# Optimization experiments

Hardware: AMD Instinct MI355X
Metric: run time of the kernel (lower is better)

## Reference

```python
import jax, jax.numpy as jnp
import numpy as np

B, S, E = 8, 4096, 768
NEG = jnp.float32(-1e30)


def setup_inputs() -> dict:
    key = jax.random.key(0)
    ks = jax.random.split(key, 9)
    full_ebd = jax.random.normal(ks[0], (B, S, E), dtype=jnp.float32)
    # first_idx in [64, S//2): end of question span (question tokens are 1..first_idx-1)
    first = jax.random.randint(ks[1], (B,), 64, S // 2)
    # second_idx in (first, S): end of context span (unused by the math but part of API)
    second = jax.random.randint(ks[2], (B,), S // 2 + 1, S)
    SEQ_idxes = jnp.stack([first, second], axis=1).astype(jnp.int64)
    w = 0.02
    Wq_w = jax.random.normal(ks[3], (E, E), dtype=jnp.float32) * w
    Wq_b = jax.random.normal(ks[4], (E,), dtype=jnp.float32) * w
    Wk_w = jax.random.normal(ks[5], (E, E), dtype=jnp.float32) * w
    Wk_b = jax.random.normal(ks[6], (E,), dtype=jnp.float32) * w
    Wv_w = jax.random.normal(ks[7], (E, E), dtype=jnp.float32) * w
    Wv_b = jax.random.normal(ks[8], (E,), dtype=jnp.float32) * w
    return {"full_ebd": full_ebd, "SEQ_idxes": SEQ_idxes,
            "Wq_w": Wq_w, "Wq_b": Wq_b, "Wk_w": Wk_w, "Wk_b": Wk_b,
            "Wv_w": Wv_w, "Wv_b": Wv_b}


def reference(full_ebd, SEQ_idxes, Wq_w, Wq_b, Wk_w, Wk_b, Wv_w, Wv_b):
    # Vectorized form of the ragged per-sample loop: queries attend to the
    # question tokens 1..first_idx-1 only; masking keys reproduces the slice.
    seq = full_ebd.shape[1]
    inv_sqrt_dk = jnp.float32(1.0 / np.sqrt(full_ebd.shape[-1]))
    Q = full_ebd @ Wq_w.T + Wq_b              # [B,S,E]
    K = full_ebd @ Wk_w.T + Wk_b              # [B,S,E]
    V = full_ebd @ Wv_w.T + Wv_b              # [B,S,E]
    first = SEQ_idxes[:, 0]                   # [B]
    j = jnp.arange(seq)
    key_mask = (j[None, :] >= 1) & (j[None, :] < first[:, None])  # [B,S]
    scores = jnp.einsum('bqe,bke->bqk', Q, K) * inv_sqrt_dk       # [B,S,S]
    scores = jnp.where(key_mask[:, None, :], scores, NEG)
    attn = jax.nn.softmax(scores, axis=-1)
    attn = attn * key_mask[:, None, :].astype(attn.dtype)  # exact zeros outside span
    H = jnp.einsum('bqk,bke->bqe', attn, V)   # [B,S,E]
    return H
```

## Files before the change

kernel.cpp:

```cpp
#include <hip/hip_runtime.h>
#include <hip/hip_bf16.h>
#include <cmath>

typedef __bf16 bf16x8 __attribute__((ext_vector_type(8)));
typedef __bf16 bf16x4 __attribute__((ext_vector_type(4)));
typedef float f32x4 __attribute__((ext_vector_type(4)));

#define GLOBAL_AS __attribute__((address_space(1)))
#define LDS_AS __attribute__((address_space(3)))

__device__ __forceinline__ void async_copy16(const void* g, void* l) {
    __builtin_amdgcn_global_load_lds((const GLOBAL_AS void*)g, (LDS_AS void*)l, 16, 0, 0);
}

__device__ inline int get_first(const int* __restrict__ seq, int b) {
    int stride = (seq[1] == 0) ? 4 : 2;
    return seq[b * stride];
}

__global__ __launch_bounds__(256) void cast_f32_bf16(const float* __restrict__ in,
                                                     __bf16* __restrict__ out, int n4) {
    int i = blockIdx.x * 256 + threadIdx.x;
    if (i >= n4) return;
    float4 v = ((const float4*)in)[i];
    bf16x4 o;
    o[0] = (__bf16)v.x; o[1] = (__bf16)v.y; o[2] = (__bf16)v.z; o[3] = (__bf16)v.w;
    ((bf16x4*)out)[i] = o;
}

__global__ __launch_bounds__(256) void cast3_f32_bf16(
    const float* __restrict__ a, const float* __restrict__ b, const float* __restrict__ c,
    __bf16* __restrict__ oa, __bf16* __restrict__ ob, __bf16* __restrict__ oc, int n4) {
    int i = blockIdx.x * 256 + threadIdx.x;
    if (i >= n4) return;
    const float* in = (blockIdx.y == 0) ? a : (blockIdx.y == 1) ? b : c;
    __bf16* out = (blockIdx.y == 0) ? oa : (blockIdx.y == 1) ? ob : oc;
    float4 v = ((const float4*)in)[i];
    bf16x4 o;
    o[0] = (__bf16)v.x; o[1] = (__bf16)v.y; o[2] = (__bf16)v.z; o[3] = (__bf16)v.w;
    ((bf16x4*)out)[i] = o;
}

__global__ __launch_bounds__(256) void zero_f32(float* __restrict__ p, int n4) {
    int i = blockIdx.x * 256 + threadIdx.x;
    if (i < n4) ((f32x4*)p)[i] = f32x4{0.f, 0.f, 0.f, 0.f};
}

template <int EPI>
__global__ __launch_bounds__(256) void gemm_bt(
    const __bf16* __restrict__ A, int lda, long strideA,
    const __bf16* __restrict__ B, int ldb, long strideB,
    const float* __restrict__ bias,
    void* __restrict__ Cv, int ldc, long strideC,
    int Kfix, const int* __restrict__ seq, int exit_mode, int k_mode,
    float cs, float* __restrict__ rowsum) {
    int z = blockIdx.z;
    int m0 = blockIdx.x * 128, n0 = blockIdx.y * 128;
    int first = seq ? get_first(seq, z) : 0;
    if (exit_mode == 1 && m0 >= first) return;
    if (exit_mode == 2 && n0 >= first) return;
    int K = k_mode ? ((first + 63) & ~63) : Kfix;

    __shared__ char As[16384];
    __shared__ char Bs[16384];

    int tid = threadIdx.x;
    int lane = tid & 63, wid = tid >> 6;
    int waveM = (wid & 1) << 6, waveN = (wid >> 1) << 6;
    int quad = lane >> 4, l16 = lane & 15;

    int r0 = tid >> 3;
    int c8 = (tid & 7) ^ (r0 & 7);
    const __bf16* Ag = A + (long)z * strideA + (long)(m0 + r0) * lda + c8 * 8;
    const __bf16* Bg = B + (long)z * strideB + (long)(n0 + r0) * ldb + c8 * 8;

    f32x4 acc[4][4] = {};
    int xorv = (l16 & 7) << 4;

    for (int k0 = 0; k0 < K; k0 += 64) {
        __syncthreads();
#pragma unroll
        for (int r = 0; r < 4; ++r) {
            async_copy16(Ag + (long)(r * 32) * lda + k0, As + (tid + r * 256) * 16);
            async_copy16(Bg + (long)(r * 32) * ldb + k0, Bs + (tid + r * 256) * 16);
        }
        __syncthreads();
#pragma unroll
        for (int s = 0; s < 2; ++s) {
            bf16x8 af[4], bfr[4];
#pragma unroll
            for (int i = 0; i < 4; ++i) {
                int chunk = (((s << 2) + quad) << 4) ^ xorv;
                af[i]  = *(const bf16x8*)(As + (waveM + i * 16 + l16) * 128 + chunk);
                bfr[i] = *(const bf16x8*)(Bs + (waveN + i * 16 + l16) * 128 + chunk);
            }
#pragma unroll
            for (int i = 0; i < 4; ++i)
#pragma unroll
                for (int j = 0; j < 4; ++j)
                    acc[i][j] = __builtin_amdgcn_mfma_f32_16x16x32_bf16(af[i], bfr[j], acc[i][j], 0, 0, 0);
        }
    }

    if (EPI == 0) {
        __bf16* C = (__bf16*)Cv + (long)z * strideC;
#pragma unroll
        for (int i = 0; i < 4; ++i) {
            int rowb = m0 + waveM + i * 16 + quad * 4;
#pragma unroll
            for (int j = 0; j < 4; ++j) {
                int col = n0 + waveN + j * 16 + l16;
                float bv_ = bias[col];
#pragma unroll
                for (int r = 0; r < 4; ++r)
                    C[(long)(rowb + r) * ldc + col] = (__bf16)(acc[i][j][r] + bv_);
            }
        }
    } else if (EPI == 1) {
        __bf16* C = (__bf16*)Cv + (long)z * strideC;
#pragma unroll
        for (int i = 0; i < 4; ++i) {
            int rowb = m0 + waveM + i * 16 + quad * 4;
#pragma unroll
            for (int j = 0; j < 4; ++j) {
                int col = n0 + waveN + j * 16 + l16;
                float bv_ = bias[col];
                bf16x4 o;
#pragma unroll
                for (int r = 0; r < 4; ++r) o[r] = (__bf16)(acc[i][j][r] + bv_);
                *(bf16x4*)&C[(long)col * ldc + rowb] = o;
            }
        }
    } else if (EPI == 2) {
        __bf16* C = (__bf16*)Cv + (long)z * strideC;
        float* rs = rowsum + (long)z * 4096;
#pragma unroll
        for (int i = 0; i < 4; ++i) {
            int rowb = m0 + waveM + i * 16 + quad * 4;
            float sum[4] = {0.f, 0.f, 0.f, 0.f};
#pragma unroll
            for (int j = 0; j < 4; ++j) {
                int col = n0 + waveN + j * 16 + l16;
                bool valid = (col >= 1) && (col < first);
#pragma unroll
                for (int r = 0; r < 4; ++r) {
                    float e = valid ? exp2f(acc[i][j][r] * cs) : 0.0f;
                    __bf16 pb = (__bf16)e;
                    C[(long)(rowb + r) * ldc + col] = pb;
                    sum[r] += (float)pb;
                }
            }
#pragma unroll
            for (int r = 0; r < 4; ++r) {
                float v = sum[r];
                v += __shfl_xor(v, 8); v += __shfl_xor(v, 4);
                v += __shfl_xor(v, 2); v += __shfl_xor(v, 1);
                if (l16 == 0) atomicAdd(&rs[rowb + r], v);
            }
        }
    } else {
        float* C = (float*)Cv + (long)z * strideC;
        const float* rs = rowsum + (long)z * 4096;
#pragma unroll
        for (int i = 0; i < 4; ++i) {
            int rowb = m0 + waveM + i * 16 + quad * 4;
            float inv[4];
#pragma unroll
            for (int r = 0; r < 4; ++r) inv[r] = 1.0f / rs[rowb + r];
#pragma unroll
            for (int j = 0; j < 4; ++j) {
                int col = n0 + waveN + j * 16 + l16;
#pragma unroll
                for (int r = 0; r < 4; ++r)
                    C[(long)(rowb + r) * ldc + col] = acc[i][j][r] * inv[r];
            }
        }
    }
}

extern "C" void kernel_launch(void* const* d_in, const int* in_sizes, int n_in,
                              void* d_out, int out_size, void* d_ws, size_t ws_size,
                              hipStream_t stream) {
    const int B = 8, S = 4096, E = 768, SK = 2048;
    const float* ebd  = (const float*)d_in[0];
    const int*   seq  = (const int*)d_in[1];
    const float* Wq_w = (const float*)d_in[2];
    const float* Wq_b = (const float*)d_in[3];
    const float* Wk_w = (const float*)d_in[4];
    const float* Wk_b = (const float*)d_in[5];
    const float* Wv_w = (const float*)d_in[6];
    const float* Wv_b = (const float*)d_in[7];
    float* out = (float*)d_out;

    char* p = (char*)d_ws;
    __bf16* ebd_bf = (__bf16*)p; p += (size_t)B * S * E * 2;
    __bf16* wq = (__bf16*)p;     p += (size_t)E * E * 2;
    __bf16* wk = (__bf16*)p;     p += (size_t)E * E * 2;
    __bf16* wv = (__bf16*)p;     p += (size_t)E * E * 2;
    __bf16* Qb = (__bf16*)p;     p += (size_t)B * S * E * 2;
    __bf16* Kb = (__bf16*)p;     p += (size_t)B * SK * E * 2;
    __bf16* VT = (__bf16*)p;     p += (size_t)B * E * SK * 2;
    __bf16* Pb = (__bf16*)p;     p += (size_t)B * S * SK * 2;
    float* rowsum = (float*)p;   p += (size_t)B * S * 4;

    zero_f32<<<B * S / 4 / 256, 256, 0, stream>>>(rowsum, B * S / 4);
    cast_f32_bf16<<<(B * S * E / 4 + 255) / 256, 256, 0, stream>>>(ebd, ebd_bf, B * S * E / 4);
    cast3_f32_bf16<<<dim3((E * E / 4 + 255) / 256, 3), 256, 0, stream>>>(
        Wq_w, Wk_w, Wv_w, wq, wk, wv, E * E / 4);

    float cs = (1.0f / sqrtf((float)E)) * 1.44269504088896f;

    gemm_bt<0><<<dim3(B * S / 128, E / 128, 1), 256, 0, stream>>>(
        ebd_bf, E, 0, wq, E, 0, Wq_b, Qb, E, 0, E, nullptr, 0, 0, 0.f, nullptr);
    gemm_bt<0><<<dim3(SK / 128, E / 128, B), 256, 0, stream>>>(
        ebd_bf, E, (long)S * E, wk, E, 0, Wk_b, Kb, E, (long)SK * E, E, seq, 1, 0, 0.f, nullptr);
    gemm_bt<1><<<dim3(SK / 128, E / 128, B), 256, 0, stream>>>(
        ebd_bf, E, (long)S * E, wv, E, 0, Wv_b, VT, SK, (long)E * SK, E, seq, 1, 0, 0.f, nullptr);
    gemm_bt<2><<<dim3(S / 128, SK / 128, B), 256, 0, stream>>>(
        Qb, E, (long)S * E, Kb, E, (long)SK * E, nullptr, Pb, SK, (long)S * SK, E, seq, 2, 0, cs, rowsum);
    gemm_bt<3><<<dim3(S / 128, E / 128, B), 256, 0, stream>>>(
        Pb, SK, (long)S * SK, VT, SK, (long)E * SK, nullptr, out, E, (long)S * E, 0, seq, 0, 1, 0.f, rowsum);
}
```

Baseline: 450.1 us.

## Add 256x256 eight-wave GEMM with interleaved staging for Q, scores and PV

```diff
diff --git a/kernel.cpp b/kernel.cpp
--- a/kernel.cpp
+++ b/kernel.cpp
@@ -12,6 +12,9 @@
 __device__ __forceinline__ void async_copy16(const void* g, void* l) {
     __builtin_amdgcn_global_load_lds((const GLOBAL_AS void*)g, (LDS_AS void*)l, 16, 0, 0);
 }
+
+#define SBAR() asm volatile("s_barrier" ::: "memory")
+#define WAITLGKM0() asm volatile("s_waitcnt lgkmcnt(0)" ::: "memory")
 
 __device__ inline int get_first(const int* __restrict__ seq, int b) {
     int stride = (seq[1] == 0) ? 4 : 2;
@@ -116,7 +119,7 @@
                     C[(long)(rowb + r) * ldc + col] = (__bf16)(acc[i][j][r] + bv_);
             }
         }
-    } else if (EPI == 1) {
+    } else {
         __bf16* C = (__bf16*)Cv + (long)z * strideC;
 #pragma unroll
         for (int i = 0; i < 4; ++i) {
@@ -131,16 +134,170 @@
                 *(bf16x4*)&C[(long)col * ldc + rowb] = o;
             }
         }
+    }
+}
+
+template <int EPI>
+__global__ __launch_bounds__(512, 2) void gemm256(
+    const __bf16* __restrict__ A, int lda, long strideA,
+    const __bf16* __restrict__ B, int ldb, long strideB,
+    const float* __restrict__ bias,
+    void* __restrict__ Cv, int ldc, long strideC,
+    int Kfix, const int* __restrict__ seq, int exit_mode, int k_mode,
+    float cs, float* __restrict__ rowsum) {
+    int z = blockIdx.z;
+    int m0 = blockIdx.x * 256, n0 = blockIdx.y * 256;
+    int first = seq ? get_first(seq, z) : 0;
+    if (exit_mode == 2 && n0 >= first) return;
+    int K = k_mode ? ((first + 63) & ~63) : Kfix;
+    int nt = K >> 6;
+
+    __shared__ char As[2][32768];
+    __shared__ char Bs[2][32768];
+
+    int tid = threadIdx.x;
+    int lane = tid & 63, wid = tid >> 6;
+    int wr = (wid >> 2) << 7;
+    int wc = (wid & 3) << 6;
+    int quad = lane >> 4, l16 = lane & 15;
+    int xr = l16 & 7;
+
+    int rg = tid >> 3;
+    int src_c8 = (tid & 7) ^ (rg & 7);
+    const __bf16* Ag = A + (long)z * strideA + (long)(m0 + rg) * lda + src_c8 * 8;
+    const __bf16* Bg = B + (long)z * strideB + (long)(n0 + rg) * ldb + src_c8 * 8;
+
+#define STAGE_A(bb, g, kk) async_copy16(Ag + (long)((g) * 64) * lda + (kk), &As[bb][(g) * 8192 + tid * 16])
+#define STAGE_B(bb, g, kk) async_copy16(Bg + (long)((g) * 64) * ldb + (kk), &Bs[bb][(g) * 8192 + tid * 16])
+#define AFRAG(base, row, s) (*(const bf16x8*)((base) + (row) * 128 + ((((s << 2) + quad) ^ xr) << 4)))
+
+    f32x4 acc[8][4] = {};
+
+    STAGE_A(0, 0, 0); STAGE_A(0, 2, 0);
+    STAGE_B(0, 0, 0); STAGE_B(0, 2, 0);
+    STAGE_B(0, 1, 0); STAGE_B(0, 3, 0);
+    STAGE_A(0, 1, 0); STAGE_A(0, 3, 0);
+    asm volatile("s_waitcnt vmcnt(2)" ::: "memory");
+    SBAR();
+
+    bf16x8 a[4][2];
+    bf16x8 bq[2][2][2];
+
+    for (int kt = 0; kt < nt; ++kt) {
+        int buf = kt & 1, nbuf = buf ^ 1;
+        int k0n = (kt + 1) << 6;
+        bool stg = (kt + 1) < nt;
+        const char* Ab = &As[buf][0];
+        const char* Bb = &Bs[buf][0];
+
+#pragma unroll
+        for (int i = 0; i < 4; ++i)
+#pragma unroll
+            for (int s = 0; s < 2; ++s)
+                a[i][s] = AFRAG(Ab, wr + i * 16 + l16, s);
+#pragma unroll
+        for (int j = 0; j < 2; ++j)
+#pragma unroll
+            for (int s = 0; s < 2; ++s)
+                bq[0][j][s] = AFRAG(Bb, wc + j * 16 + l16, s);
+        if (stg) { STAGE_A(nbuf, 0, k0n); STAGE_A(nbuf, 2, k0n); STAGE_B(nbuf, 0, k0n); STAGE_B(nbuf, 2, k0n); }
+        SBAR();
+        WAITLGKM0();
+        __builtin_amdgcn_s_setprio(1);
+#pragma unroll
+        for (int i = 0; i < 4; ++i)
+#pragma unroll
+            for (int j = 0; j < 2; ++j)
+#pragma unroll
+                for (int s = 0; s < 2; ++s)
+                    acc[i][j] = __builtin_amdgcn_mfma_f32_16x16x32_bf16(a[i][s], bq[0][j][s], acc[i][j], 0, 0, 0);
+        __builtin_amdgcn_s_setprio(0);
+        SBAR();
+
+#pragma unroll
+        for (int j = 0; j < 2; ++j)
+#pragma unroll
+            for (int s = 0; s < 2; ++s)
+                bq[1][j][s] = AFRAG(Bb, wc + 32 + j * 16 + l16, s);
+        if (stg) {
+            STAGE_B(nbuf, 1, k0n); STAGE_B(nbuf, 3, k0n);
+            STAGE_A(nbuf, 1, k0n); STAGE_A(nbuf, 3, k0n);
+            asm volatile("s_waitcnt vmcnt(8)" ::: "memory");
+        } else {
+            asm volatile("s_waitcnt vmcnt(0)" ::: "memory");
+        }
+        SBAR();
+        WAITLGKM0();
+        __builtin_amdgcn_s_setprio(1);
+#pragma unroll
+        for (int i = 0; i < 4; ++i)
+#pragma unroll
+            for (int j = 0; j < 2; ++j)
+#pragma unroll
+                for (int s = 0; s < 2; ++s)
+                    acc[i][2 + j] = __builtin_amdgcn_mfma_f32_16x16x32_bf16(a[i][s], bq[1][j][s], acc[i][2 + j], 0, 0, 0);
+        __builtin_amdgcn_s_setprio(0);
+        SBAR();
+
+#pragma unroll
+        for (int i = 0; i < 4; ++i)
+#pragma unroll
+            for (int s = 0; s < 2; ++s)
+                a[i][s] = AFRAG(Ab, wr + 64 + i * 16 + l16, s);
+        SBAR();
+        WAITLGKM0();
+        __builtin_amdgcn_s_setprio(1);
+#pragma unroll
+        for (int i = 0; i < 4; ++i)
+#pragma unroll
+            for (int j = 0; j < 2; ++j)
+#pragma unroll
+                for (int s = 0; s < 2; ++s)
+                    acc[4 + i][j] = __builtin_amdgcn_mfma_f32_16x16x32_bf16(a[i][s], bq[0][j][s], acc[4 + i][j], 0, 0, 0);
+        __builtin_amdgcn_s_setprio(0);
+        SBAR();
+
+        asm volatile("s_waitcnt vmcnt(2)" ::: "memory");
+        SBAR();
+        __builtin_amdgcn_s_setprio(1);
+#pragma unroll
+        for (int i = 0; i < 4; ++i)
+#pragma unroll
+            for (int j = 0; j < 2; ++j)
+#pragma unroll
+                for (int s = 0; s < 2; ++s)
+                    acc[4 + i][2 + j] = __builtin_amdgcn_mfma_f32_16x16x32_bf16(a[i][s], bq[1][j][s], acc[4 + i][2 + j], 0, 0, 0);
+        __builtin_amdgcn_s_setprio(0);
+        SBAR();
+    }
+#undef STAGE_A
+#undef STAGE_B
+#undef AFRAG
+
+    if (EPI == 0) {
+        __bf16* C = (__bf16*)Cv + (long)z * strideC;
+#pragma unroll
+        for (int i = 0; i < 8; ++i) {
+            int rowb = m0 + wr + i * 16 + quad * 4;
+#pragma unroll
+            for (int j = 0; j < 4; ++j) {
+                int col = n0 + wc + j * 16 + l16;
+                float bv_ = bias[col];
+#pragma unroll
+                for (int r = 0; r < 4; ++r)
+                    C[(long)(rowb + r) * ldc + col] = (__bf16)(acc[i][j][r] + bv_);
+            }
+        }
     } else if (EPI == 2) {
         __bf16* C = (__bf16*)Cv + (long)z * strideC;
-        float* rs = rowsum + (long)z * 4096;
-#pragma unroll
-        for (int i = 0; i < 4; ++i) {
-            int rowb = m0 + waveM + i * 16 + quad * 4;
+        float* rsum = rowsum + (long)z * 4096;
+#pragma unroll
+        for (int i = 0; i < 8; ++i) {
+            int rowb = m0 + wr + i * 16 + quad * 4;
             float sum[4] = {0.f, 0.f, 0.f, 0.f};
 #pragma unroll
             for (int j = 0; j < 4; ++j) {
-                int col = n0 + waveN + j * 16 + l16;
+                int col = n0 + wc + j * 16 + l16;
                 bool valid = (col >= 1) && (col < first);
 #pragma unroll
                 for (int r = 0; r < 4; ++r) {
@@ -155,21 +312,21 @@
                 float v = sum[r];
                 v += __shfl_xor(v, 8); v += __shfl_xor(v, 4);
                 v += __shfl_xor(v, 2); v += __shfl_xor(v, 1);
-                if (l16 == 0) atomicAdd(&rs[rowb + r], v);
+                if (l16 == 0) atomicAdd(&rsum[rowb + r], v);
             }
         }
     } else {
         float* C = (float*)Cv + (long)z * strideC;
-        const float* rs = rowsum + (long)z * 4096;
-#pragma unroll
-        for (int i = 0; i < 4; ++i) {
-            int rowb = m0 + waveM + i * 16 + quad * 4;
+        const float* rsum = rowsum + (long)z * 4096;
+#pragma unroll
+        for (int i = 0; i < 8; ++i) {
+            int rowb = m0 + wr + i * 16 + quad * 4;
             float inv[4];
 #pragma unroll
-            for (int r = 0; r < 4; ++r) inv[r] = 1.0f / rs[rowb + r];
-#pragma unroll
-            for (int j = 0; j < 4; ++j) {
-                int col = n0 + waveN + j * 16 + l16;
+            for (int r = 0; r < 4; ++r) inv[r] = 1.0f / rsum[rowb + r];
+#pragma unroll
+            for (int j = 0; j < 4; ++j) {
+                int col = n0 + wc + j * 16 + l16;
 #pragma unroll
                 for (int r = 0; r < 4; ++r)
                     C[(long)(rowb + r) * ldc + col] = acc[i][j][r] * inv[r];
@@ -210,14 +367,14 @@
 
     float cs = (1.0f / sqrtf((float)E)) * 1.44269504088896f;
 
-    gemm_bt<0><<<dim3(B * S / 128, E / 128, 1), 256, 0, stream>>>(
+    gemm256<0><<<dim3(B * S / 256, E / 256, 1), 512, 0, stream>>>(
         ebd_bf, E, 0, wq, E, 0, Wq_b, Qb, E, 0, E, nullptr, 0, 0, 0.f, nullptr);
     gemm_bt<0><<<dim3(SK / 128, E / 128, B), 256, 0, stream>>>(
         ebd_bf, E, (long)S * E, wk, E, 0, Wk_b, Kb, E, (long)SK * E, E, seq, 1, 0, 0.f, nullptr);
     gemm_bt<1><<<dim3(SK / 128, E / 128, B), 256, 0, stream>>>(
         ebd_bf, E, (long)S * E, wv, E, 0, Wv_b, VT, SK, (long)E * SK, E, seq, 1, 0, 0.f, nullptr);
-    gemm_bt<2><<<dim3(S / 128, SK / 128, B), 256, 0, stream>>>(
+    gemm256<2><<<dim3(S / 256, SK / 256, B), 512, 0, stream>>>(
         Qb, E, (long)S * E, Kb, E, (long)SK * E, nullptr, Pb, SK, (long)S * SK, E, seq, 2, 0, cs, rowsum);
-    gemm_bt<3><<<dim3(S / 128, E / 128, B), 256, 0, stream>>>(
+    gemm256<3><<<dim3(S / 256, E / 256, B), 512, 0, stream>>>(
         Pb, SK, (long)S * SK, VT, SK, (long)E * SK, nullptr, out, E, (long)S * E, 0, seq, 0, 1, 0.f, rowsum);
 }
```

Measured after the change: 469.4 us. 4.3% more time.
